# Kernel optimization log

Hardware: AMD Instinct MI355X
Metric: run time of the kernel (lower is better)

The kernel has to match this reference:

```python
import jax, jax.numpy as jnp
import numpy as np

EPS = 1e-5

def layer_norm(x, w):
    mu = x.mean(-1, keepdims=True)
    var = x.var(-1, keepdims=True)
    return (x - mu) * jax.lax.rsqrt(var + EPS) * w

def multihead_norm(x, w):
    # x: (B,S,NH,DH) -> group norm per head, elementwise weight over NH*DH features
    mu = x.mean(-1, keepdims=True)
    var = x.var(-1, keepdims=True)
    xn = (x - mu) * jax.lax.rsqrt(var + EPS)
    B, S, NH, DH = x.shape
    return xn.reshape(B, S, NH * DH) * w

def causal_conv1d(x, W, b):
    # x: (B,S,C), W: (C,K) depthwise causal conv, bias b: (C,)
    C, K = W.shape
    ker = W.T[:, None, :]  # (K,1,C) in WIO layout
    y = jax.lax.conv_general_dilated(x, ker, (1,), [(K - 1, 0)],
                                     dimension_numbers=('NWC', 'WIO', 'NWC'),
                                     feature_group_count=C)
    return y + b

def headwise_linear(x, W):
    # block-diagonal linear; W: (nblocks, out, in)
    nb, o, i = W.shape
    B, S, F = x.shape
    y = jnp.einsum('bsni,noi->bsno', x.reshape(B, S, nb, i), W)
    return y.reshape(B, S, nb * o)

def mlstm_block(x, ln_w, up_W, conv_W, conv_b, q_W, k_W, v_W, ig_W, ig_b, fg_W, fg_b, on_w, skip, down_W):
    B, S, E = x.shape
    I = up_W.shape[1] // 2
    NH = ig_W.shape[0]
    DH = I // NH
    xn = layer_norm(x, ln_w)
    up = xn @ up_W                       # (B,S,2I)
    xm, z = up[..., :I], up[..., I:]
    xc = jax.nn.silu(causal_conv1d(xm, conv_W, conv_b))
    q = headwise_linear(xc, q_W)
    k = headwise_linear(xc, k_W)
    v = headwise_linear(xm, v_W)        # values come from the pre-conv branch
    gin = jnp.concatenate([q, k, v], -1)  # (B,S,3I)
    ig = (gin @ ig_W.T + ig_b).transpose(0, 2, 1)  # (B,NH,S)
    fg = (gin @ fg_W.T + fg_b).transpose(0, 2, 1)
    qh = q.reshape(B, S, NH, DH).transpose(0, 2, 1, 3)
    kh = k.reshape(B, S, NH, DH).transpose(0, 2, 1, 3)
    vh = v.reshape(B, S, NH, DH).transpose(0, 2, 1, 3)
    # parallel stabilized mLSTM (matrix memory)
    logf = jax.nn.log_sigmoid(fg)
    cs = jnp.concatenate([jnp.zeros_like(logf[..., :1]), jnp.cumsum(logf, -1)], -1)  # (B,NH,S+1)
    lf = cs[..., 1:, None] - cs[..., None, 1:]   # (B,NH,S,S): sum of log f over (t, s]
    mask = jnp.tril(jnp.ones((S, S), bool))
    log_D = jnp.where(mask, lf + ig[:, :, None, :], -jnp.inf)
    max_log_D = log_D.max(-1, keepdims=True)
    D = jnp.exp(log_D - max_log_D)
    qk = jnp.einsum('bhsd,bhtd->bhst', qh, kh) * (DH ** -0.5)
    C = qk * D
    normalizer = jnp.maximum(jnp.abs(C.sum(-1, keepdims=True)), jnp.exp(-max_log_D))
    h = jnp.einsum('bhst,bhtd->bhsd', C / (normalizer + 1e-6), vh)
    h = multihead_norm(h.transpose(0, 2, 1, 3), on_w)  # (B,S,I)
    h = (h + skip * xc) * jax.nn.silu(z)
    return x + h @ down_W

def slstm_block(x, ln_w, conv_W, conv_b, gates_W, R, bias, gn_w, ffn_ln_w, ffn_up_W, ffn_down_W):
    B, S, E = x.shape
    NH, DH = R.shape[0], R.shape[1]
    xn = layer_norm(x, ln_w)
    xc = jax.nn.silu(causal_conv1d(xn, conv_W, conv_b))
    xh = xn.reshape(B, S, NH, DH)
    xch = xc.reshape(B, S, NH, DH)
    i_pre = jnp.einsum('bsnd,nod->bsno', xch, gates_W[0])  # i,f gates see conv branch
    f_pre = jnp.einsum('bsnd,nod->bsno', xch, gates_W[1])
    z_pre = jnp.einsum('bsnd,nod->bsno', xh, gates_W[2])
    o_pre = jnp.einsum('bsnd,nod->bsno', xh, gates_W[3])
    gx = jnp.stack([i_pre, f_pre, z_pre, o_pre], 3) + bias  # (B,S,NH,4,DH)
    def step(carry, g):
        h, c, n, m = carry
        raw = g + jnp.einsum('bnd,ndg->bng', h, R).reshape(B, NH, 4, DH)
        ir, fr, zr, og = raw[:, :, 0], raw[:, :, 1], raw[:, :, 2], raw[:, :, 3]
        logfplusm = m + jax.nn.log_sigmoid(fr)
        m_new = jnp.maximum(ir, logfplusm)
        i = jnp.exp(ir - m_new)
        f = jnp.exp(logfplusm - m_new)
        c_new = f * c + i * jnp.tanh(zr)
        n_new = f * n + i
        h_new = jax.nn.sigmoid(og) * c_new / n_new
        return (h_new, c_new, n_new, m_new), h_new
    z0 = jnp.zeros((B, NH, DH), x.dtype)
    _, hs = jax.lax.scan(step, (z0, z0, z0, z0), gx.transpose(1, 0, 2, 3, 4))
    y = multihead_norm(hs.transpose(1, 0, 2, 3), gn_w)  # (B,S,E)
    x = x + y
    xn2 = layer_norm(x, ffn_ln_w)
    gpre, upp = jnp.split(xn2 @ ffn_up_W, 2, -1)
    return x + (jax.nn.gelu(gpre, approximate=False) * upp) @ ffn_down_W

def forward(x, m_ln_w, m_up_W, m_conv_W, m_conv_b, m_q_W, m_k_W, m_v_W, m_ig_W, m_ig_b, m_fg_W, m_fg_b, m_outnorm_w, m_skip, m_down_W, s_ln_w, s_conv_W, s_conv_b, s_gates_W, s_R, s_bias, s_gn_w, s_ffn_ln_w, s_ffn_up_W, s_ffn_down_W, post_norm_w, fc_W, fc_b):
    mi = 0
    for blk in range(7):  # slstm_at=[1]
        if blk == 1:
            x = slstm_block(x, s_ln_w, s_conv_W, s_conv_b, s_gates_W, s_R, s_bias, s_gn_w, s_ffn_ln_w, s_ffn_up_W, s_ffn_down_W)
        else:
            x = mlstm_block(x, m_ln_w[mi], m_up_W[mi], m_conv_W[mi], m_conv_b[mi], m_q_W[mi], m_k_W[mi], m_v_W[mi], m_ig_W[mi], m_ig_b[mi], m_fg_W[mi], m_fg_b[mi], m_outnorm_w[mi], m_skip[mi], m_down_W[mi])
            mi += 1
    x = layer_norm(x, post_norm_w)
    return x[:, -1, :] @ fc_W + fc_b

def setup_inputs():
    key = jax.random.key(0)
    ks = jax.random.split(key, 18)
    B, S, E = 16, 512, 128
    I, NH = 256, 4
    DHs = E // NH
    FF = 192
    NB = 6
    r = lambda k, shape, sc: jax.random.normal(k, shape, jnp.float32) * sc
    return dict(
        x=r(ks[0], (B, S, E), 1.0),
        m_ln_w=jnp.ones((NB, E), jnp.float32),
        m_up_W=r(ks[1], (NB, E, 2 * I), E ** -0.5),
        m_conv_W=r(ks[2], (NB, I, 4), 0.3),
        m_conv_b=jnp.zeros((NB, I), jnp.float32),
        m_q_W=r(ks[3], (NB, 64, 4, 4), 0.5),
        m_k_W=r(ks[4], (NB, 64, 4, 4), 0.5),
        m_v_W=r(ks[5], (NB, 64, 4, 4), 0.5),
        m_ig_W=r(ks[6], (NB, NH, 3 * I), 0.1 * (3 * I) ** -0.5),
        m_ig_b=r(ks[7], (NB, NH), 0.5),
        m_fg_W=r(ks[8], (NB, NH, 3 * I), 0.1 * (3 * I) ** -0.5),
        m_fg_b=r(ks[9], (NB, NH), 1.0) + 3.0,
        m_outnorm_w=jnp.ones((NB, I), jnp.float32),
        m_skip=jnp.ones((NB, I), jnp.float32),
        m_down_W=r(ks[10], (NB, I, E), I ** -0.5),
        s_ln_w=jnp.ones((E,), jnp.float32),
        s_conv_W=r(ks[11], (E, 4), 0.3),
        s_conv_b=jnp.zeros((E,), jnp.float32),
        s_gates_W=r(ks[12], (4, NH, DHs, DHs), DHs ** -0.5),
        s_R=r(ks[13], (NH, DHs, 4 * DHs), 0.5 * DHs ** -0.5),
        s_bias=r(ks[14], (NH, 4, DHs), 0.1),
        s_gn_w=jnp.ones((E,), jnp.float32),
        s_ffn_ln_w=jnp.ones((E,), jnp.float32),
        s_ffn_up_W=r(ks[15], (E, 2 * FF), E ** -0.5),
        s_ffn_down_W=r(ks[16], (FF, E), FF ** -0.5),
        post_norm_w=jnp.ones((E,), jnp.float32),
        fc_W=r(ks[17], (E, 1), E ** -0.5),
        fc_b=jnp.zeros((1,), jnp.float32),
    )

def reference(x, m_ln_w, m_up_W, m_conv_W, m_conv_b, m_q_W, m_k_W, m_v_W, m_ig_W, m_ig_b, m_fg_W, m_fg_b, m_outnorm_w, m_skip, m_down_W, s_ln_w, s_conv_W, s_conv_b, s_gates_W, s_R, s_bias, s_gn_w, s_ffn_ln_w, s_ffn_up_W, s_ffn_down_W, post_norm_w, fc_W, fc_b):
    return forward(x, m_ln_w, m_up_W, m_conv_W, m_conv_b, m_q_W, m_k_W, m_v_W, m_ig_W, m_ig_b, m_fg_W, m_fg_b, m_outnorm_w, m_skip, m_down_W, s_ln_w, s_conv_W, s_conv_b, s_gates_W, s_R, s_bias, s_gn_w, s_ffn_ln_w, s_ffn_up_W, s_ffn_down_W, post_norm_w, fc_W, fc_b)
```

## Files before the change

### kernel.cpp

```cpp
#include <hip/hip_runtime.h>
#include <cstddef>

constexpr int B = 16, S = 512, E = 128, I = 256, DHm = 64;
constexpr int BS = B * S;

typedef _Float16 half8 __attribute__((ext_vector_type(8)));
typedef _Float16 half4 __attribute__((ext_vector_type(4)));
typedef float f32x4 __attribute__((ext_vector_type(4)));

template <int BM, int BN, bool ADD, int FUSE>
__global__ void __launch_bounds__(256) gemm2(const float* __restrict__ A,
                                             const float* __restrict__ W,
                                             const float* __restrict__ lnw,
                                             float* __restrict__ C, int M, int N, int K) {
  constexpr int TM = BM / 16, TN = BN / 16;
  __shared__ float As[32][BM];
  __shared__ float Ws[32][BN];
  __shared__ float smu[BM], srr[BM];
  const int n0 = blockIdx.x * BN, m0 = blockIdx.y * BM;
  const int tid = threadIdx.x;
  const int tr = tid >> 4, tc = tid & 15;
  if constexpr (FUSE == 1) {
    constexpr int TPR = 256 / BM;
    int row = tid / TPR, q = tid % TPR;
    const float* ap = A + (size_t)(m0 + row) * K + q * (128 / TPR);
    float s1 = 0.f, s2 = 0.f;
#pragma unroll
    for (int i = 0; i < 128 / TPR / 4; i++) {
      float4 v = *(const float4*)(ap + i * 4);
      s1 += v.x + v.y + v.z + v.w;
      s2 += v.x * v.x + v.y * v.y + v.z * v.z + v.w * v.w;
    }
#pragma unroll
    for (int m = 1; m < TPR; m <<= 1) { s1 += __shfl_xor(s1, m); s2 += __shfl_xor(s2, m); }
    if (q == 0) {
      float mu = s1 * (1.f / 128);
      float var = s2 * (1.f / 128) - mu * mu;
      smu[row] = mu;
      srr[row] = rsqrtf(var + 1e-5f);
    }
    __syncthreads();
  }
  float acc[TM][TN] = {};
  for (int k0 = 0; k0 < K; k0 += 32) {
#pragma unroll
    for (int i = 0; i < BM / 32; i++) {
      int lin = tid + i * 256;
      int mm = lin >> 3, kq = lin & 7;
      float4 a4;
      if constexpr (FUSE == 2) {
        const float* ap = A + (size_t)(m0 + mm) * 384 + k0 + kq * 4;
        float4 g4 = *(const float4*)ap;
        float4 u4 = *(const float4*)(ap + 192);
        a4.x = 0.5f * g4.x * (1.f + erff(g4.x * 0.70710678118f)) * u4.x;
        a4.y = 0.5f * g4.y * (1.f + erff(g4.y * 0.70710678118f)) * u4.y;
        a4.z = 0.5f * g4.z * (1.f + erff(g4.z * 0.70710678118f)) * u4.z;
        a4.w = 0.5f * g4.w * (1.f + erff(g4.w * 0.70710678118f)) * u4.w;
      } else {
        a4 = *(const float4*)(A + (size_t)(m0 + mm) * K + k0 + kq * 4);
      }
      if constexpr (FUSE == 1) {
        float mu = smu[mm], rr = srr[mm];
        float4 wl = *(const float4*)(lnw + k0 + kq * 4);
        a4.x = (a4.x - mu) * rr * wl.x;
        a4.y = (a4.y - mu) * rr * wl.y;
        a4.z = (a4.z - mu) * rr * wl.z;
        a4.w = (a4.w - mu) * rr * wl.w;
      }
      int col = (mm ^ (kq * 4)) & (BM - 1);
      As[kq * 4 + 0][col] = a4.x;
      As[kq * 4 + 1][col] = a4.y;
      As[kq * 4 + 2][col] = a4.z;
      As[kq * 4 + 3][col] = a4.w;
    }
#pragma unroll
    for (int i = 0; i < BN / 32; i++) {
      int lin = tid + i * 256;
      int kk = lin / (BN / 4), nq = lin % (BN / 4);
      *(float4*)&Ws[kk][nq * 4] = *(const float4*)(W + (size_t)(k0 + kk) * N + n0 + nq * 4);
    }
    __syncthreads();
#pragma unroll
    for (int k = 0; k < 32; k++) {
      float av[TM], bv[TN];
      const int xs = (k >> 2) * 4;
      *(float4*)&av[0] = *(const float4*)&As[k][((tr * 4) ^ xs) & (BM - 1)];
      if constexpr (TM == 8)
        *(float4*)&av[4] = *(const float4*)&As[k][(((tr * 4) ^ xs) & (BM - 1)) + 64];
      *(float4*)&bv[0] = *(const float4*)&Ws[k][tc * 4];
      if constexpr (TN == 8) *(float4*)&bv[4] = *(const float4*)&Ws[k][tc * 4 + 64];
#pragma unroll
      for (int ii = 0; ii < TM; ii++)
#pragma unroll
        for (int jj = 0; jj < TN; jj++) acc[ii][jj] += av[ii] * bv[jj];
    }
    __syncthreads();
  }
#pragma unroll
  for (int ii = 0; ii < TM; ii++) {
    int row = m0 + tr * 4 + (ii & 3) + ((ii >= 4) ? 64 : 0);
    float* cp = C + (size_t)row * N + n0 + tc * 4;
    float4 o = make_float4(acc[ii][0], acc[ii][1], acc[ii][2], acc[ii][3]);
    if (ADD) {
      float4 c4 = *(const float4*)cp;
      o.x += c4.x; o.y += c4.y; o.z += c4.z; o.w += c4.w;
    }
    *(float4*)cp = o;
    if constexpr (TN == 8) {
      float4 o2 = make_float4(acc[ii][4], acc[ii][5], acc[ii][6], acc[ii][7]);
      if (ADD) {
        float4 c4 = *(const float4*)(cp + 64);
        o2.x += c4.x; o2.y += c4.y; o2.z += c4.z; o2.w += c4.w;
      }
      *(float4*)(cp + 64) = o2;
    }
  }
}

__global__ void __launch_bounds__(256) mlstm_mid_kernel(
    const float* __restrict__ UP, const float* __restrict__ conv_W,
    const float* __restrict__ conv_b, const float* __restrict__ qW,
    const float* __restrict__ kW, const float* __restrict__ vW,
    const float* __restrict__ igW, const float* __restrict__ igb,
    const float* __restrict__ fgW, const float* __restrict__ fgb,
    float* __restrict__ XC, float* __restrict__ Q, float* __restrict__ Kb,
    float* __restrict__ V, float* __restrict__ IG, float* __restrict__ FG) {
  __shared__ float xcl[I], xml[I], qkvl[768];
  __shared__ float red[32];
  int r = blockIdx.x, t = threadIdx.x;
  int s = r & (S - 1);
  const float* xr = UP + (size_t)r * 512 + t;
  float4 w4 = *(const float4*)(conv_W + t * 4);
  float x0 = xr[0];
  float acc = conv_b[t] + x0 * w4.w;
  if (s >= 1) acc += xr[-512] * w4.z;
  if (s >= 2) acc += xr[-1024] * w4.y;
  if (s >= 3) acc += xr[-1536] * w4.x;
  float xc = acc / (1.f + __expf(-acc));
  xcl[t] = xc;
  xml[t] = x0;
  XC[(size_t)r * I + t] = xc;
  __syncthreads();
  int n = t >> 2, o = t & 3;
  const float* qw = qW + n * 16 + o * 4;
  const float* kw = kW + n * 16 + o * 4;
  const float* vw = vW + n * 16 + o * 4;
  float q = 0, k = 0, v = 0;
#pragma unroll
  for (int i = 0; i < 4; i++) {
    float xcv = xcl[n * 4 + i], xmv = xml[n * 4 + i];
    q += xcv * qw[i]; k += xcv * kw[i]; v += xmv * vw[i];
  }
  Q[(size_t)r * I + t] = q;
  Kb[(size_t)r * I + t] = k;
  V[(size_t)r * I + t] = v;
  qkvl[t] = q; qkvl[256 + t] = k; qkvl[512 + t] = v;
  __syncthreads();
  float ai[4] = {}, af[4] = {};
#pragma unroll
  for (int j = 0; j < 3; j++) {
    int c = t + j * 256;
    float g = qkvl[c];
#pragma unroll
    for (int h = 0; h < 4; h++) {
      ai[h] += g * igW[h * 768 + c];
      af[h] += g * fgW[h * 768 + c];
    }
  }
#pragma unroll
  for (int m = 32; m; m >>= 1)
#pragma unroll
    for (int h = 0; h < 4; h++) {
      ai[h] += __shfl_xor(ai[h], m);
      af[h] += __shfl_xor(af[h], m);
    }
  int wv = t >> 6;
  if ((t & 63) == 0) {
#pragma unroll
    for (int h = 0; h < 4; h++) { red[wv * 8 + h] = ai[h]; red[wv * 8 + 4 + h] = af[h]; }
  }
  __syncthreads();
  if (t < 8) {
    float sum = red[t] + red[8 + t] + red[16 + t] + red[24 + t];
    int b = r >> 9, srow = r & (S - 1);
    int h = t & 3;
    if (t < 4) IG[((size_t)(b * 4 + h)) * S + srow] = sum + igb[h];
    else FG[((size_t)(b * 4 + h)) * S + srow] = sum + fgb[h];
  }
}

__device__ __forceinline__ int swz(int row, int col) {
  return (row * 64 + col) ^ ((row & 7) << 3);
}
struct h3s { _Float16 a, b, c; };
__device__ __forceinline__ h3s split3(float x) {
  h3s r;
  r.a = (_Float16)x;
  float t = x - (float)r.a;
  r.b = (_Float16)t;
  t -= (float)r.b;
  r.c = (_Float16)t;
  return r;
}

__global__ void __launch_bounds__(256) attn_mfma_kernel(
    const float* __restrict__ Q, const float* __restrict__ Kb, const float* __restrict__ V,
    const float* __restrict__ IG, const float* __restrict__ FG,
    const float* __restrict__ XC, const float* __restrict__ UP,
    const float* __restrict__ onw, const float* __restrict__ skip,
    float* __restrict__ HF) {
  __shared__ _Float16 K1[4096], K2[4096], K3[4096];
  __shared__ _Float16 V1[4096], V2[4096], V3[4096];
  __shared__ _Float16 W1[4096], W2[4096], W3[4096];
  __shared__ float A_l[512], M_l[512], F_l[512];
  int bid = blockIdx.x;
  int st = bid & 7, bh = bid >> 3;
  int b = bh >> 2, h = bh & 3;
  int s0 = st * 64;
  int tid = threadIdx.x;
  const float* Qg = Q + ((size_t)b * S) * I + h * DHm;
  const float* Kg = Kb + ((size_t)b * S) * I + h * DHm;
  const float* Vg = V + ((size_t)b * S) * I + h * DHm;

  const int lane = tid & 63, w = tid >> 6;
  const int sband = w * 16;
  const int fr = lane & 15, fg = lane >> 4;

  if (tid < 64) {
    int l = tid;
    const float* ig = IG + (size_t)bh * S;
    const float* fgp = FG + (size_t)bh * S;
    float lfc[8], av[8], amx[8];
    float cs = 0;
#pragma unroll
    for (int j = 0; j < 8; j++) {
      float f = fgp[l * 8 + j];
      cs += fminf(f, 0.f) - log1pf(__expf(-fabsf(f)));
      lfc[j] = cs;
    }
    float tot = cs, inc = tot;
#pragma unroll
    for (int off = 1; off < 64; off <<= 1) {
      float yv = __shfl_up(inc, off);
      if (l >= off) inc += yv;
    }
    float excl = inc - tot;
    float pm = -1e30f;
#pragma unroll
    for (int j = 0; j < 8; j++) {
      float CSj = excl + lfc[j];
      av[j] = ig[l * 8 + j] - CSj;
      pm = fmaxf(pm, av[j]);
      amx[j] = pm;
      lfc[j] = CSj;
    }
    float incm = pm;
#pragma unroll
    for (int off = 1; off < 64; off <<= 1) {
      float yv = __shfl_up(incm, off);
      if (l >= off) incm = fmaxf(incm, yv);
    }
    float exclm = __shfl_up(incm, 1);
    if (l == 0) exclm = -1e30f;
#pragma unroll
    for (int j = 0; j < 8; j++) {
      float Mj = fmaxf(exclm, amx[j]);
      A_l[l * 8 + j] = av[j];
      M_l[l * 8 + j] = Mj;
      F_l[l * 8 + j] = __expf(-(lfc[j] + Mj));
    }
  }

  half8 aq1[2], aq2[2], aq3[2];
  {
    const float* qrow = Qg + (size_t)(s0 + sband + fr) * I;
#pragma unroll
    for (int c = 0; c < 2; c++) {
      float4 qa = *(const float4*)(qrow + c * 32 + fg * 8);
      float4 qb = *(const float4*)(qrow + c * 32 + fg * 8 + 4);
      float qv[8] = {qa.x, qa.y, qa.z, qa.w, qb.x, qb.y, qb.z, qb.w};
#pragma unroll
      for (int j = 0; j < 8; j++) {
        h3s sp = split3(qv[j]);
        aq1[c][j] = sp.a; aq2[c][j] = sp.b; aq3[c][j] = sp.c;
      }
    }
  }
  __syncthreads();
  float msl[4];
#pragma unroll
  for (int r = 0; r < 4; r++) msl[r] = M_l[s0 + sband + fg * 4 + r];

  f32x4 hacc[4] = {};
  float csp[4] = {};

  for (int tt = 0; tt <= st; tt++) {
    int t0 = tt * 64;
    __syncthreads();
#pragma unroll
    for (int i = 0; i < 4; i++) {
      int lin = tid + i * 256;
      int t = lin >> 4, dq = (lin & 15) * 4;
      float4 kv = *(const float4*)(Kg + (size_t)(t0 + t) * I + dq);
      const float ka[4] = {kv.x, kv.y, kv.z, kv.w};
      half4 k1, k2, k3;
#pragma unroll
      for (int j = 0; j < 4; j++) {
        h3s sp = split3(ka[j]);
        k1[j] = sp.a; k2[j] = sp.b; k3[j] = sp.c;
      }
      *(half4*)&K1[swz(t, dq)] = k1;
      *(half4*)&K2[swz(t, dq)] = k2;
      *(half4*)&K3[swz(t, dq)] = k3;
      float4 vv = *(const float4*)(Vg + (size_t)(t0 + t) * I + dq);
      const float va[4] = {vv.x, vv.y, vv.z, vv.w};
#pragma unroll
      for (int j = 0; j < 4; j++) {
        h3s sp = split3(va[j]);
        V1[swz(dq + j, t)] = sp.a;
        V2[swz(dq + j, t)] = sp.b;
        V3[swz(dq + j, t)] = sp.c;
      }
    }
    __syncthreads();
#pragma unroll
    for (int ct = 0; ct < 4; ct++) {
      f32x4 sacc = {};
#pragma unroll
      for (int c = 0; c < 2; c++) {
        half8 b1 = *(const half8*)&K1[swz(ct * 16 + fr, c * 32 + fg * 8)];
        half8 b2 = *(const half8*)&K2[swz(ct * 16 + fr, c * 32 + fg * 8)];
        half8 b3 = *(const half8*)&K3[swz(ct * 16 + fr, c * 32 + fg * 8)];
        sacc = __builtin_amdgcn_mfma_f32_16x16x32_f16(aq3[c], b1, sacc, 0, 0, 0);
        sacc = __builtin_amdgcn_mfma_f32_16x16x32_f16(aq2[c], b2, sacc, 0, 0, 0);
        sacc = __builtin_amdgcn_mfma_f32_16x16x32_f16(aq1[c], b3, sacc, 0, 0, 0);
        sacc = __builtin_amdgcn_mfma_f32_16x16x32_f16(aq2[c], b1, sacc, 0, 0, 0);
        sacc = __builtin_amdgcn_mfma_f32_16x16x32_f16(aq1[c], b2, sacc, 0, 0, 0);
        sacc = __builtin_amdgcn_mfma_f32_16x16x32_f16(aq1[c], b1, sacc, 0, 0, 0);
      }
      int tg = t0 + ct * 16 + fr;
      float ea = A_l[tg];
#pragma unroll
      for (int r = 0; r < 4; r++) {
        int sl = sband + fg * 4 + r;
        float wv = 0.f;
        if (tg <= s0 + sl) wv = sacc[r] * 0.125f * __expf(ea - msl[r]);
        csp[r] += wv;
        h3s sp = split3(wv);
        W1[swz(sl, ct * 16 + fr)] = sp.a;
        W2[swz(sl, ct * 16 + fr)] = sp.b;
        W3[swz(sl, ct * 16 + fr)] = sp.c;
      }
    }
#pragma unroll
    for (int kc = 0; kc < 2; kc++) {
      half8 w1 = *(const half8*)&W1[swz(sband + fr, kc * 32 + fg * 8)];
      half8 w2 = *(const half8*)&W2[swz(sband + fr, kc * 32 + fg * 8)];
      half8 w3 = *(const half8*)&W3[swz(sband + fr, kc * 32 + fg * 8)];
#pragma unroll
      for (int dt = 0; dt < 4; dt++) {
        half8 v1 = *(const half8*)&V1[swz(dt * 16 + fr, kc * 32 + fg * 8)];
        half8 v2 = *(const half8*)&V2[swz(dt * 16 + fr, kc * 32 + fg * 8)];
        half8 v3 = *(const half8*)&V3[swz(dt * 16 + fr, kc * 32 + fg * 8)];
        hacc[dt] = __builtin_amdgcn_mfma_f32_16x16x32_f16(w3, v1, hacc[dt], 0, 0, 0);
        hacc[dt] = __builtin_amdgcn_mfma_f32_16x16x32_f16(w2, v2, hacc[dt], 0, 0, 0);
        hacc[dt] = __builtin_amdgcn_mfma_f32_16x16x32_f16(w1, v3, hacc[dt], 0, 0, 0);
        hacc[dt] = __builtin_amdgcn_mfma_f32_16x16x32_f16(w2, v1, hacc[dt], 0, 0, 0);
        hacc[dt] = __builtin_amdgcn_mfma_f32_16x16x32_f16(w1, v2, hacc[dt], 0, 0, 0);
        hacc[dt] = __builtin_amdgcn_mfma_f32_16x16x32_f16(w1, v1, hacc[dt], 0, 0, 0);
      }
    }
  }
#pragma unroll
  for (int m = 1; m < 16; m <<= 1)
#pragma unroll
    for (int r = 0; r < 4; r++) csp[r] += __shfl_xor(csp[r], m);
  float on4[4], sk4[4];
#pragma unroll
  for (int dt = 0; dt < 4; dt++) {
    on4[dt] = onw[h * DHm + dt * 16 + fr];
    sk4[dt] = skip[h * DHm + dt * 16 + fr];
  }
#pragma unroll
  for (int r = 0; r < 4; r++) {
    int sl = sband + fg * 4 + r;
    size_t row = (size_t)b * S + s0 + sl;
    float Fv = F_l[s0 + sl];
    float inv = 1.f / (fmaxf(fabsf(csp[r]), Fv) + 1e-6f);
    float hv[4], s1 = 0.f, s2 = 0.f;
#pragma unroll
    for (int dt = 0; dt < 4; dt++) {
      hv[dt] = hacc[dt][r] * inv;
      s1 += hv[dt];
      s2 += hv[dt] * hv[dt];
    }
#pragma unroll
    for (int m = 1; m < 16; m <<= 1) { s1 += __shfl_xor(s1, m); s2 += __shfl_xor(s2, m); }
    float mu = s1 * (1.f / 64), var = s2 * (1.f / 64) - mu * mu;
    float rr = rsqrtf(var + 1e-5f);
#pragma unroll
    for (int dt = 0; dt < 4; dt++) {
      int col = h * DHm + dt * 16 + fr;
      float xc = XC[row * I + col];
      float zv = UP[row * (2 * I) + I + col];
      float hn = (hv[dt] - mu) * rr * on4[dt];
      HF[row * I + col] = (hn + sk4[dt] * xc) * (zv / (1.f + __expf(-zv)));
    }
  }
}

__global__ void __launch_bounds__(512) slstm_pre_kernel(
    const float* __restrict__ X, const float* __restrict__ lnw,
    const float* __restrict__ conv_W, const float* __restrict__ conv_b,
    const float* __restrict__ gW, const float* __restrict__ bias,
    float* __restrict__ GX) {
  __shared__ float xnl[4][128], xcl[128];
  __shared__ float redS[8], redQ[8];
  int r = blockIdx.x, t = threadIdx.x;
  int s = r & (S - 1);
  int b0 = r - s;
  int rr = t >> 7, cc = t & 127;
  int sr = s - 3 + rr;
  int grow = b0 + (sr > 0 ? sr : 0);
  float x = X[(size_t)grow * E + cc];
  float s1 = x, s2 = x * x;
#pragma unroll
  for (int m = 32; m; m >>= 1) { s1 += __shfl_xor(s1, m); s2 += __shfl_xor(s2, m); }
  int wv = t >> 6;
  if ((t & 63) == 0) { redS[wv] = s1; redQ[wv] = s2; }
  __syncthreads();
  float fs1 = redS[rr * 2] + redS[rr * 2 + 1];
  float fs2 = redQ[rr * 2] + redQ[rr * 2 + 1];
  float mu = fs1 * (1.f / 128);
  float var = fs2 * (1.f / 128) - mu * mu;
  xnl[rr][cc] = (x - mu) * rsqrtf(var + 1e-5f) * lnw[cc];
  __syncthreads();
  if (t < 128) {
    float4 w4 = *(const float4*)(conv_W + t * 4);
    float acc = conv_b[t] + xnl[3][t] * w4.w;
    if (s >= 1) acc += xnl[2][t] * w4.z;
    if (s >= 2) acc += xnl[1][t] * w4.y;
    if (s >= 3) acc += xnl[0][t] * w4.x;
    xcl[t] = acc / (1.f + __expf(-acc));
  }
  __syncthreads();
  int n = t >> 7, g = (t >> 5) & 3, o = t & 31;
  const float* src = (g < 2) ? (xcl + n * 32) : (xnl[3] + n * 32);
  const float* wp = gW + (((size_t)g * 4 + n) * 32 + o) * 32;
  float acc = bias[n * 128 + g * 32 + o];
#pragma unroll
  for (int d = 0; d < 32; d++) acc += src[d] * wp[d];
  GX[(size_t)r * 512 + t] = acc;
}

__global__ void __launch_bounds__(128) slstm_scan8(const float* __restrict__ GX,
                                                   const float* __restrict__ R,
                                                   float* __restrict__ HS) {
  constexpr int CH = 16, NCH = S / CH;
  __shared__ float ring[2][CH][128];
  int blk = blockIdx.x;
  int b = blk >> 2, n = blk & 3;
  int tid = threadIdx.x;
  int wv = tid >> 6, l = tid & 63;
  const float* gxp = GX + ((size_t)b * S) * 512 + n * 128;

  float R0[32], R1[32];
  float h_own = 0.f, c = 0.f, nn = 0.f, m = 0.f;
  if (wv == 0) {
#pragma unroll
    for (int d = 0; d < 32; d++) {
      R0[d] = R[((size_t)(n * 32 + d)) * 128 + l];
      R1[d] = R[((size_t)(n * 32 + d)) * 128 + 64 + l];
    }
  } else {
    float v0[CH], v1[CH];
#pragma unroll
    for (int j = 0; j < CH; j++) {
      v0[j] = gxp[(size_t)j * 512 + l];
      v1[j] = gxp[(size_t)j * 512 + 64 + l];
    }
#pragma unroll
    for (int j = 0; j < CH; j++) {
      ring[0][j][l] = v0[j];
      ring[0][j][64 + l] = v1[j];
    }
  }
  __syncthreads();

  for (int ck = 0; ck < NCH; ck++) {
    if (wv == 1) {
      if (ck + 1 < NCH) {
        const float* src = gxp + (size_t)(ck + 1) * CH * 512;
        float v0[CH], v1[CH];
#pragma unroll
        for (int j = 0; j < CH; j++) {
          v0[j] = src[(size_t)j * 512 + l];
          v1[j] = src[(size_t)j * 512 + 64 + l];
        }
        int pb = (ck + 1) & 1;
#pragma unroll
        for (int j = 0; j < CH; j++) {
          ring[pb][j][l] = v0[j];
          ring[pb][j][64 + l] = v1[j];
        }
      }
    } else {
      int cb = ck & 1;
#pragma unroll
      for (int j = 0; j < CH; j++) {
        float g0 = ring[cb][j][l];
        float g1 = ring[cb][j][64 + l];
        float r0p0 = g0, r0p1 = 0.f, r0p2 = 0.f, r0p3 = 0.f;
        float r1p0 = g1, r1p1 = 0.f, r1p2 = 0.f, r1p3 = 0.f;
#pragma unroll
        for (int d = 0; d < 32; d += 4) {
          float hv0 = __shfl(h_own, d);
          float hv1 = __shfl(h_own, d + 1);
          float hv2 = __shfl(h_own, d + 2);
          float hv3 = __shfl(h_own, d + 3);
          r0p0 += hv0 * R0[d];     r1p0 += hv0 * R1[d];
          r0p1 += hv1 * R0[d + 1]; r1p1 += hv1 * R1[d + 1];
          r0p2 += hv2 * R0[d + 2]; r1p2 += hv2 * R1[d + 2];
          r0p3 += hv3 * R0[d + 3]; r1p3 += hv3 * R1[d + 3];
        }
        float raw0 = (r0p0 + r0p1) + (r0p2 + r0p3);
        float raw1 = (r1p0 + r1p1) + (r1p2 + r1p3);
        float fr = __shfl_down(raw0, 32);
        float og = __shfl_down(raw1, 32);
        float ir = raw0, zr = raw1;
        float lsf = fminf(fr, 0.f) - __logf(1.f + __expf(-fabsf(fr)));
        float lfm = m + lsf;
        float mn = fmaxf(ir, lfm);
        float iv = __expf(ir - mn), fv = __expf(lfm - mn);
        float th = 1.f - 2.f / (__expf(2.f * zr) + 1.f);
        c = fv * c + iv * th;
        nn = fv * nn + iv;
        m = mn;
        float hv = (c / nn) / (1.f + __expf(-og));
        h_own = hv;
        int s = ck * CH + j;
        if (l < 32) HS[((size_t)(b * S + s)) * E + n * 32 + l] = hv;
      }
    }
    __syncthreads();
  }
}

__global__ void gnorm_add_kernel(const float* __restrict__ HS, const float* __restrict__ gnw,
                                 float* __restrict__ X) {
  int r = blockIdx.x, t = threadIdx.x;
  float v = HS[(size_t)r * E + t];
  float s1 = v, s2 = v * v;
#pragma unroll
  for (int m = 16; m; m >>= 1) { s1 += __shfl_xor(s1, m, 32); s2 += __shfl_xor(s2, m, 32); }
  float mu = s1 * (1.f / 32), var = s2 * (1.f / 32) - mu * mu;
  X[(size_t)r * E + t] += (v - mu) * rsqrtf(var + 1e-5f) * gnw[t];
}

__global__ void head_kernel(const float* __restrict__ X, const float* __restrict__ pw,
                            const float* __restrict__ fcW, const float* __restrict__ fcb,
                            float* __restrict__ out) {
  int b = blockIdx.x, l = threadIdx.x;
  const float* xr = X + ((size_t)(b * S + S - 1)) * E;
  float2 v = *(const float2*)(xr + l * 2);
  float s1 = v.x + v.y, s2 = v.x * v.x + v.y * v.y;
#pragma unroll
  for (int m = 32; m; m >>= 1) { s1 += __shfl_xor(s1, m); s2 += __shfl_xor(s2, m); }
  float mu = s1 * (1.f / E), var = s2 * (1.f / E) - mu * mu;
  float rr = rsqrtf(var + 1e-5f);
  float2 wv = *(const float2*)(pw + l * 2);
  float2 fw = *(const float2*)(fcW + l * 2);
  float acc = (v.x - mu) * rr * wv.x * fw.x + (v.y - mu) * rr * wv.y * fw.y;
#pragma unroll
  for (int m = 32; m; m >>= 1) acc += __shfl_xor(acc, m);
  if (l == 0) out[b] = acc + fcb[0];
}

extern "C" void kernel_launch(void* const* d_in, const int* in_sizes, int n_in, void* d_out,
                              int out_size, void* d_ws, size_t ws_size, hipStream_t stream) {
  const float* in_x = (const float*)d_in[0];
  const float* m_ln_w = (const float*)d_in[1];
  const float* m_up_W = (const float*)d_in[2];
  const float* m_conv_W = (const float*)d_in[3];
  const float* m_conv_b = (const float*)d_in[4];
  const float* m_q_W = (const float*)d_in[5];
  const float* m_k_W = (const float*)d_in[6];
  const float* m_v_W = (const float*)d_in[7];
  const float* m_ig_W = (const float*)d_in[8];
  const float* m_ig_b = (const float*)d_in[9];
  const float* m_fg_W = (const float*)d_in[10];
  const float* m_fg_b = (const float*)d_in[11];
  const float* m_on_w = (const float*)d_in[12];
  const float* m_skip = (const float*)d_in[13];
  const float* m_down_W = (const float*)d_in[14];
  const float* s_ln_w = (const float*)d_in[15];
  const float* s_conv_W = (const float*)d_in[16];
  const float* s_conv_b = (const float*)d_in[17];
  const float* s_gates_W = (const float*)d_in[18];
  const float* s_R = (const float*)d_in[19];
  const float* s_bias = (const float*)d_in[20];
  const float* s_gn_w = (const float*)d_in[21];
  const float* s_ffn_ln_w = (const float*)d_in[22];
  const float* s_ffn_up_W = (const float*)d_in[23];
  const float* s_ffn_down_W = (const float*)d_in[24];
  const float* post_norm_w = (const float*)d_in[25];
  const float* fc_W = (const float*)d_in[26];
  const float* fc_b = (const float*)d_in[27];

  float* ws = (float*)d_ws;
  float* X = ws;
  float* XN = X + 1048576;
  float* UP = XN + 1048576;
  float* XC = UP + 4194304;
  float* Qb = XC + 2097152;
  float* Kb = Qb + 2097152;
  float* Vb = Kb + 2097152;
  float* Hb = Vb + 2097152;
  float* IGb = Hb + 2097152;
  float* FGb = IGb + 32768;

  hipMemcpyAsync(X, in_x, (size_t)BS * E * sizeof(float), hipMemcpyDeviceToDevice, stream);

  int mi = 0;
  for (int blk = 0; blk < 7; blk++) {
    if (blk == 1) {
      slstm_pre_kernel<<<BS, 512, 0, stream>>>(X, s_ln_w, s_conv_W, s_conv_b, s_gates_W,
                                               s_bias, UP);
      slstm_scan8<<<64, 128, 0, stream>>>(UP, s_R, Hb);
      gnorm_add_kernel<<<BS, E, 0, stream>>>(Hb, s_gn_w, X);
      gemm2<64, 128, false, 1><<<dim3(3, 128), 256, 0, stream>>>(X, s_ffn_up_W, s_ffn_ln_w,
                                                                 UP, BS, 384, 128);
      gemm2<64, 64, true, 2><<<dim3(2, 128), 256, 0, stream>>>(UP, s_ffn_down_W, nullptr, X,
                                                               BS, 128, 192);
    } else {
      const float* ln_w = m_ln_w + (size_t)mi * E;
      const float* up_W = m_up_W + (size_t)mi * E * 512;
      const float* conv_W = m_conv_W + (size_t)mi * I * 4;
      const float* conv_b = m_conv_b + (size_t)mi * I;
      const float* q_W = m_q_W + (size_t)mi * 1024;
      const float* k_W = m_k_W + (size_t)mi * 1024;
      const float* v_W = m_v_W + (size_t)mi * 1024;
      const float* ig_W = m_ig_W + (size_t)mi * 3072;
      const float* ig_b = m_ig_b + (size_t)mi * 4;
      const float* fg_W = m_fg_W + (size_t)mi * 3072;
      const float* fg_b = m_fg_b + (size_t)mi * 4;
      const float* on_w = m_on_w + (size_t)mi * I;
      const float* skipv = m_skip + (size_t)mi * I;
      const float* down_W = m_down_W + (size_t)mi * I * E;

      gemm2<64, 128, false, 1><<<dim3(4, 128), 256, 0, stream>>>(X, up_W, ln_w, UP, BS, 512,
                                                                 128);
      mlstm_mid_kernel<<<BS, 256, 0, stream>>>(UP, conv_W, conv_b, q_W, k_W, v_W, ig_W, ig_b,
                                               fg_W, fg_b, XC, Qb, Kb, Vb, IGb, FGb);
      attn_mfma_kernel<<<512, 256, 0, stream>>>(Qb, Kb, Vb, IGb, FGb, XC, UP, on_w, skipv,
                                                Hb);
      gemm2<64, 64, true, 0><<<dim3(2, 128), 256, 0, stream>>>(Hb, down_W, nullptr, X, BS,
                                                               128, 256);
      mi++;
    }
  }
  head_kernel<<<B, 64, 0, stream>>>(X, post_norm_w, fc_W, fc_b, (float*)d_out);
}
```

Baseline: 1.340 ms.

## Replace FP32 SIMT GEMMs with split-FP16 MFMA GEMM kernel

Replaces the scalar FP32 tiled GEMM with a 64x64 tile kernel that splits each FP32 operand into two FP16 parts and accumulates three MFMA 16x16x32 products, which approximates FP32 accuracy. The aim is to move the up/down projection and FFN GEMMs from vector ALUs onto matrix cores. The fused layernorm and GELU-gating prologues are kept. The cost is extra conversion work, a transposed scalar store of W into LDS, and a slight loss of precision from dropping the low-by-low term.

```diff
diff --git a/kernel.cpp b/kernel.cpp
--- a/kernel.cpp
+++ b/kernel.cpp
@@ -8,48 +8,72 @@
 typedef _Float16 half4 __attribute__((ext_vector_type(4)));
 typedef float f32x4 __attribute__((ext_vector_type(4)));
 
-template <int BM, int BN, bool ADD, int FUSE>
-__global__ void __launch_bounds__(256) gemm2(const float* __restrict__ A,
+__device__ __forceinline__ int swz(int row, int col) {
+  return (row * 64 + col) ^ ((row & 7) << 3);
+}
+struct h3s { _Float16 a, b, c; };
+__device__ __forceinline__ h3s split3(float x) {
+  h3s r;
+  r.a = (_Float16)x;
+  float t = x - (float)r.a;
+  r.b = (_Float16)t;
+  t -= (float)r.b;
+  r.c = (_Float16)t;
+  return r;
+}
+struct h2s { _Float16 a, b; };
+__device__ __forceinline__ h2s split2(float x) {
+  h2s r;
+  r.a = (_Float16)x;
+  r.b = (_Float16)(x - (float)r.a);
+  return r;
+}
+
+template <int K, bool ADD, int FUSE>
+__global__ void __launch_bounds__(256) gemm3(const float* __restrict__ A,
                                              const float* __restrict__ W,
                                              const float* __restrict__ lnw,
-                                             float* __restrict__ C, int M, int N, int K) {
-  constexpr int TM = BM / 16, TN = BN / 16;
-  __shared__ float As[32][BM];
-  __shared__ float Ws[32][BN];
-  __shared__ float smu[BM], srr[BM];
-  const int n0 = blockIdx.x * BN, m0 = blockIdx.y * BM;
+                                             float* __restrict__ C, int N, int astride) {
+  __shared__ _Float16 A1[4096], A2[4096];
+  __shared__ _Float16 B1[4096], B2[4096];
+  __shared__ float smu[64], srr[64];
+  const int n0 = blockIdx.x * 64, m0 = blockIdx.y * 64;
   const int tid = threadIdx.x;
-  const int tr = tid >> 4, tc = tid & 15;
+  const int lane = tid & 63, w = tid >> 6;
+  const int sband = w * 16;
+  const int fr = lane & 15, fg = lane >> 4;
+
   if constexpr (FUSE == 1) {
-    constexpr int TPR = 256 / BM;
-    int row = tid / TPR, q = tid % TPR;
-    const float* ap = A + (size_t)(m0 + row) * K + q * (128 / TPR);
+    int row = tid >> 2, q = tid & 3;
+    const float* ap = A + (size_t)(m0 + row) * astride + q * 32;
     float s1 = 0.f, s2 = 0.f;
 #pragma unroll
-    for (int i = 0; i < 128 / TPR / 4; i++) {
+    for (int i = 0; i < 8; i++) {
       float4 v = *(const float4*)(ap + i * 4);
       s1 += v.x + v.y + v.z + v.w;
       s2 += v.x * v.x + v.y * v.y + v.z * v.z + v.w * v.w;
     }
-#pragma unroll
-    for (int m = 1; m < TPR; m <<= 1) { s1 += __shfl_xor(s1, m); s2 += __shfl_xor(s2, m); }
+    s1 += __shfl_xor(s1, 1); s2 += __shfl_xor(s2, 1);
+    s1 += __shfl_xor(s1, 2); s2 += __shfl_xor(s2, 2);
     if (q == 0) {
       float mu = s1 * (1.f / 128);
       float var = s2 * (1.f / 128) - mu * mu;
       smu[row] = mu;
       srr[row] = rsqrtf(var + 1e-5f);
     }
+  }
+
+  f32x4 acc[4] = {};
+#pragma unroll
+  for (int k0 = 0; k0 < K; k0 += 64) {
     __syncthreads();
-  }
-  float acc[TM][TN] = {};
-  for (int k0 = 0; k0 < K; k0 += 32) {
-#pragma unroll
-    for (int i = 0; i < BM / 32; i++) {
+#pragma unroll
+    for (int i = 0; i < 4; i++) {
       int lin = tid + i * 256;
-      int mm = lin >> 3, kq = lin & 7;
+      int mm = lin >> 4, kq = (lin & 15) * 4;
       float4 a4;
       if constexpr (FUSE == 2) {
-        const float* ap = A + (size_t)(m0 + mm) * 384 + k0 + kq * 4;
+        const float* ap = A + (size_t)(m0 + mm) * astride + k0 + kq;
         float4 g4 = *(const float4*)ap;
         float4 u4 = *(const float4*)(ap + 192);
         a4.x = 0.5f * g4.x * (1.f + erff(g4.x * 0.70710678118f)) * u4.x;
@@ -57,62 +81,67 @@
         a4.z = 0.5f * g4.z * (1.f + erff(g4.z * 0.70710678118f)) * u4.z;
         a4.w = 0.5f * g4.w * (1.f + erff(g4.w * 0.70710678118f)) * u4.w;
       } else {
-        a4 = *(const float4*)(A + (size_t)(m0 + mm) * K + k0 + kq * 4);
+        a4 = *(const float4*)(A + (size_t)(m0 + mm) * astride + k0 + kq);
       }
       if constexpr (FUSE == 1) {
         float mu = smu[mm], rr = srr[mm];
-        float4 wl = *(const float4*)(lnw + k0 + kq * 4);
+        float4 wl = *(const float4*)(lnw + k0 + kq);
         a4.x = (a4.x - mu) * rr * wl.x;
         a4.y = (a4.y - mu) * rr * wl.y;
         a4.z = (a4.z - mu) * rr * wl.z;
         a4.w = (a4.w - mu) * rr * wl.w;
       }
-      int col = (mm ^ (kq * 4)) & (BM - 1);
-      As[kq * 4 + 0][col] = a4.x;
-      As[kq * 4 + 1][col] = a4.y;
-      As[kq * 4 + 2][col] = a4.z;
-      As[kq * 4 + 3][col] = a4.w;
-    }
-#pragma unroll
-    for (int i = 0; i < BN / 32; i++) {
+      const float av[4] = {a4.x, a4.y, a4.z, a4.w};
+      half4 h1, h2;
+#pragma unroll
+      for (int j = 0; j < 4; j++) {
+        h2s sp = split2(av[j]);
+        h1[j] = sp.a; h2[j] = sp.b;
+      }
+      *(half4*)&A1[swz(mm, kq)] = h1;
+      *(half4*)&A2[swz(mm, kq)] = h2;
+    }
+#pragma unroll
+    for (int i = 0; i < 4; i++) {
       int lin = tid + i * 256;
-      int kk = lin / (BN / 4), nq = lin % (BN / 4);
-      *(float4*)&Ws[kk][nq * 4] = *(const float4*)(W + (size_t)(k0 + kk) * N + n0 + nq * 4);
+      int kk = lin >> 4, nq = (lin & 15) * 4;
+      float4 w4 = *(const float4*)(W + (size_t)(k0 + kk) * N + n0 + nq);
+      const float wv[4] = {w4.x, w4.y, w4.z, w4.w};
+#pragma unroll
+      for (int j = 0; j < 4; j++) {
+        h2s sp = split2(wv[j]);
+        B1[swz(nq + j, kk)] = sp.a;
+        B2[swz(nq + j, kk)] = sp.b;
+      }
     }
     __syncthreads();
-#pragma unroll
-    for (int k = 0; k < 32; k++) {
-      float av[TM], bv[TN];
-      const int xs = (k >> 2) * 4;
-      *(float4*)&av[0] = *(const float4*)&As[k][((tr * 4) ^ xs) & (BM - 1)];
-      if constexpr (TM == 8)
-        *(float4*)&av[4] = *(const float4*)&As[k][(((tr * 4) ^ xs) & (BM - 1)) + 64];
-      *(float4*)&bv[0] = *(const float4*)&Ws[k][tc * 4];
-      if constexpr (TN == 8) *(float4*)&bv[4] = *(const float4*)&Ws[k][tc * 4 + 64];
-#pragma unroll
-      for (int ii = 0; ii < TM; ii++)
-#pragma unroll
-        for (int jj = 0; jj < TN; jj++) acc[ii][jj] += av[ii] * bv[jj];
-    }
-    __syncthreads();
-  }
-#pragma unroll
-  for (int ii = 0; ii < TM; ii++) {
-    int row = m0 + tr * 4 + (ii & 3) + ((ii >= 4) ? 64 : 0);
-    float* cp = C + (size_t)row * N + n0 + tc * 4;
-    float4 o = make_float4(acc[ii][0], acc[ii][1], acc[ii][2], acc[ii][3]);
-    if (ADD) {
-      float4 c4 = *(const float4*)cp;
-      o.x += c4.x; o.y += c4.y; o.z += c4.z; o.w += c4.w;
-    }
-    *(float4*)cp = o;
-    if constexpr (TN == 8) {
-      float4 o2 = make_float4(acc[ii][4], acc[ii][5], acc[ii][6], acc[ii][7]);
-      if (ADD) {
-        float4 c4 = *(const float4*)(cp + 64);
-        o2.x += c4.x; o2.y += c4.y; o2.z += c4.z; o2.w += c4.w;
-      }
-      *(float4*)(cp + 64) = o2;
+    half8 a1g0 = *(const half8*)&A1[swz(sband + fr, fg * 8)];
+    half8 a1g1 = *(const half8*)&A1[swz(sband + fr, 32 + fg * 8)];
+    half8 a2g0 = *(const half8*)&A2[swz(sband + fr, fg * 8)];
+    half8 a2g1 = *(const half8*)&A2[swz(sband + fr, 32 + fg * 8)];
+#pragma unroll
+    for (int ct = 0; ct < 4; ct++) {
+      half8 b1g0 = *(const half8*)&B1[swz(ct * 16 + fr, fg * 8)];
+      half8 b1g1 = *(const half8*)&B1[swz(ct * 16 + fr, 32 + fg * 8)];
+      half8 b2g0 = *(const half8*)&B2[swz(ct * 16 + fr, fg * 8)];
+      half8 b2g1 = *(const half8*)&B2[swz(ct * 16 + fr, 32 + fg * 8)];
+      acc[ct] = __builtin_amdgcn_mfma_f32_16x16x32_f16(a2g0, b1g0, acc[ct], 0, 0, 0);
+      acc[ct] = __builtin_amdgcn_mfma_f32_16x16x32_f16(a1g0, b2g0, acc[ct], 0, 0, 0);
+      acc[ct] = __builtin_amdgcn_mfma_f32_16x16x32_f16(a1g0, b1g0, acc[ct], 0, 0, 0);
+      acc[ct] = __builtin_amdgcn_mfma_f32_16x16x32_f16(a2g1, b1g1, acc[ct], 0, 0, 0);
+      acc[ct] = __builtin_amdgcn_mfma_f32_16x16x32_f16(a1g1, b2g1, acc[ct], 0, 0, 0);
+      acc[ct] = __builtin_amdgcn_mfma_f32_16x16x32_f16(a1g1, b1g1, acc[ct], 0, 0, 0);
+    }
+  }
+#pragma unroll
+  for (int ct = 0; ct < 4; ct++) {
+#pragma unroll
+    for (int r = 0; r < 4; r++) {
+      int row = m0 + sband + fg * 4 + r;
+      int col = n0 + ct * 16 + fr;
+      float v = acc[ct][r];
+      if (ADD) v += C[(size_t)row * N + col];
+      C[(size_t)row * N + col] = v;
     }
   }
 }
@@ -187,20 +216,6 @@
     if (t < 4) IG[((size_t)(b * 4 + h)) * S + srow] = sum + igb[h];
     else FG[((size_t)(b * 4 + h)) * S + srow] = sum + fgb[h];
   }
-}
-
-__device__ __forceinline__ int swz(int row, int col) {
-  return (row * 64 + col) ^ ((row & 7) << 3);
-}
-struct h3s { _Float16 a, b, c; };
-__device__ __forceinline__ h3s split3(float x) {
-  h3s r;
-  r.a = (_Float16)x;
-  float t = x - (float)r.a;
-  r.b = (_Float16)t;
-  t -= (float)r.b;
-  r.c = (_Float16)t;
-  return r;
 }
 
 __global__ void __launch_bounds__(256) attn_mfma_kernel(
@@ -628,10 +643,10 @@
                                                s_bias, UP);
       slstm_scan8<<<64, 128, 0, stream>>>(UP, s_R, Hb);
       gnorm_add_kernel<<<BS, E, 0, stream>>>(Hb, s_gn_w, X);
-      gemm2<64, 128, false, 1><<<dim3(3, 128), 256, 0, stream>>>(X, s_ffn_up_W, s_ffn_ln_w,
-                                                                 UP, BS, 384, 128);
-      gemm2<64, 64, true, 2><<<dim3(2, 128), 256, 0, stream>>>(UP, s_ffn_down_W, nullptr, X,
-                                                               BS, 128, 192);
+      gemm3<128, false, 1><<<dim3(6, 128), 256, 0, stream>>>(X, s_ffn_up_W, s_ffn_ln_w, UP,
+                                                             384, 128);
+      gemm3<192, true, 2><<<dim3(2, 128), 256, 0, stream>>>(UP, s_ffn_down_W, nullptr, X,
+                                                            128, 384);
     } else {
       const float* ln_w = m_ln_w + (size_t)mi * E;
       const float* up_W = m_up_W + (size_t)mi * E * 512;
@@ -648,14 +663,12 @@
       const float* skipv = m_skip + (size_t)mi * I;
       const float* down_W = m_down_W + (size_t)mi * I * E;
 
-      gemm2<64, 128, false, 1><<<dim3(4, 128), 256, 0, stream>>>(X, up_W, ln_w, UP, BS, 512,
-                                                                 128);
+      gemm3<128, false, 1><<<dim3(8, 128), 256, 0, stream>>>(X, up_W, ln_w, UP, 512, 128);
       mlstm_mid_kernel<<<BS, 256, 0, stream>>>(UP, conv_W, conv_b, q_W, k_W, v_W, ig_W, ig_b,
                                                fg_W, fg_b, XC, Qb, Kb, Vb, IGb, FGb);
       attn_mfma_kernel<<<512, 256, 0, stream>>>(Qb, Kb, Vb, IGb, FGb, XC, UP, on_w, skipv,
                                                 Hb);
-      gemm2<64, 64, true, 0><<<dim3(2, 128), 256, 0, stream>>>(Hb, down_W, nullptr, X, BS,
-                                                               128, 256);
+      gemm3<256, true, 0><<<dim3(2, 128), 256, 0, stream>>>(Hb, down_W, nullptr, X, 128, 256);
       mi++;
     }
   }
```

Result: faster. 1.283 ms (-4.3%).
